# Kernel tuning notes

Measured on AMD Instinct MI355X. Metric: run time of the kernel, lower is better.

Reference implementation:

```python
import jax, jax.numpy as jnp
import numpy as np

PAD_IDX = 1  # matches init_kwargs pad_idx
TLEN, BATCH, D_IN = 50, 16, 512
SRC_LEN, VOCAB, CVOCAB = 200, 20000, 20400


def setup_inputs() -> dict:
    key = jax.random.key(0)
    k1, k2, k3, k4, k5, k6, k7 = jax.random.split(key, 7)
    hidden = jax.random.normal(k1, (TLEN, BATCH, D_IN), dtype=jnp.float32)
    attn = jax.random.uniform(k2, (TLEN, BATCH, SRC_LEN), dtype=jnp.float32)
    # src_map is a sparse one-hot indicator: each source position maps to one extended-vocab id
    src_ids = jax.random.randint(k3, (SRC_LEN, BATCH), 0, CVOCAB)
    src_map = jax.nn.one_hot(src_ids, CVOCAB, dtype=jnp.float32)  # (src_len, batch, cvocab)
    s = 1.0 / np.sqrt(D_IN)
    W = jax.random.uniform(k4, (VOCAB, D_IN), dtype=jnp.float32, minval=-s, maxval=s)
    b = jax.random.uniform(k5, (VOCAB,), dtype=jnp.float32, minval=-s, maxval=s)
    Wc = jax.random.uniform(k6, (1, D_IN), dtype=jnp.float32, minval=-s, maxval=s)
    bc = jax.random.uniform(k7, (1,), dtype=jnp.float32, minval=-s, maxval=s)
    return {"hidden": hidden, "attn": attn, "src_map": src_map, "W": W, "b": b, "Wc": Wc, "bc": bc}


def reference(hidden, attn, src_map, W, b, Wc, bc):
    tlen, batch, _ = hidden.shape
    src_len, _, cvocab = src_map.shape
    logits = jnp.einsum('tbd,vd->tbv', hidden, W) + b            # (tlen, batch, vocab)
    # faithful to torch: logits[:, pad_idx] = -inf (indexes the batch dim!)
    logits = logits.at[:, PAD_IDX, :].set(-jnp.inf)
    prob = jax.nn.softmax(logits, axis=1)                        # softmax over dim 1, as in source
    p_copy = jax.nn.sigmoid(jnp.einsum('tbd,od->tbo', hidden, Wc) + bc)  # (tlen, batch, 1)
    out_prob = prob * (1.0 - p_copy)                             # (tlen, batch, vocab)
    mul_attn = attn * p_copy                                     # (tlen, batch, src_len)
    # bmm over batch with one-hot src_map: effectively a scatter-add into extended vocab
    copy_prob = jnp.einsum('tbs,sbv->tbv', mul_attn, src_map)    # (tlen, batch, cvocab)
    # faithful to the split/stack/transpose permutation in the source
    flat = copy_prob.reshape(tlen * batch, cvocab)
    copy_prob = flat.reshape(batch, tlen, cvocab).swapaxes(0, 1) # (tlen, batch, cvocab)
    copy_prob = copy_prob.at[:, :, :out_prob.shape[2]].add(out_prob)
    return copy_prob
```

## Files before the change

kernel.cpp:

```cpp
#include <hip/hip_runtime.h>
#include <cstdint>
#include <cstddef>

#define TLEN    50
#define BATCH   16
#define D_IN    512
#define SRC_LEN 200
#define VOCAB   20000
#define CVOCAB  20400

typedef __bf16 bf16x8 __attribute__((ext_vector_type(8)));
typedef float  f32x4  __attribute__((ext_vector_type(4)));

#define GEMM_BLOCKS 625
#define ZERO_BLOCKS 40
#define SCAN_BLOCKS (SRC_LEN * BATCH)
#define NT 128
#define APAD 8

__global__ __launch_bounds__(256)
void pc_kernel(const float* __restrict__ hidden,
               const float* __restrict__ Wc,
               const float* __restrict__ bc,
               float* __restrict__ pc)
{
    const int row  = blockIdx.x * 4 + (threadIdx.x >> 6);
    const int lane = threadIdx.x & 63;
    const float* h = hidden + (size_t)row * D_IN + lane * 8;
    float4 h0 = *(const float4*)(h);
    float4 h1 = *(const float4*)(h + 4);
    float4 w0 = *(const float4*)(Wc + lane * 8);
    float4 w1 = *(const float4*)(Wc + lane * 8 + 4);
    float s = h0.x*w0.x + h0.y*w0.y + h0.z*w0.z + h0.w*w0.w
            + h1.x*w1.x + h1.y*w1.y + h1.z*w1.z + h1.w*w1.w;
    #pragma unroll
    for (int o = 1; o < 64; o <<= 1) s += __shfl_xor(s, o);
    if (lane == 0) pc[row] = 1.0f / (1.0f + __expf(-(s + bc[0])));
}

__global__ __launch_bounds__(NT)
void fused_main(const float* __restrict__ hidden,
                const float* __restrict__ src_map,
                const float* __restrict__ W,
                const float* __restrict__ pc,
                float* __restrict__ out,
                int* __restrict__ src_ids)
{
    const int bid = blockIdx.x;
    const int tid = threadIdx.x;

    if (bid < GEMM_BLOCKS) {
        __shared__ __bf16 Alds[2][BATCH][D_IN + APAD];

        const int lane = tid & 63;
        const int wv   = tid >> 6;
        const int l15  = lane & 15;
        const int q    = lane >> 4;
        const int colbase = bid * 32 + wv * 16;

        bf16x8 bfrag[16];
        {
            const float* wrow = W + (size_t)(colbase + l15) * D_IN + q * 8;
            #pragma unroll
            for (int c = 0; c < 16; ++c) {
                float4 f0 = *(const float4*)(wrow + c * 32);
                float4 f1 = *(const float4*)(wrow + c * 32 + 4);
                bf16x8 bf;
                bf[0] = (__bf16)f0.x; bf[1] = (__bf16)f0.y;
                bf[2] = (__bf16)f0.z; bf[3] = (__bf16)f0.w;
                bf[4] = (__bf16)f1.x; bf[5] = (__bf16)f1.y;
                bf[6] = (__bf16)f1.z; bf[7] = (__bf16)f1.w;
                bfrag[c] = bf;
            }
            #pragma unroll
            for (int c = 0; c < 16; ++c) {
                f32x4 t = *(f32x4*)&bfrag[c];
                asm volatile("" : "+v"(t));
                bfrag[c] = *(bf16x8*)&t;
            }
        }

        auto stage = [&](int t, int buf) {
            #pragma unroll
            for (int i = 0; i < 16; ++i) {
                float4 v4 = *(const float4*)(hidden + ((size_t)t * BATCH + i) * D_IN + tid * 4);
                __bf16* dst = &Alds[buf][i][tid * 4];
                dst[0] = (__bf16)v4.x; dst[1] = (__bf16)v4.y;
                dst[2] = (__bf16)v4.z; dst[3] = (__bf16)v4.w;
            }
        };

        stage(0, 0);

        for (int t = 0; t < TLEN; ++t) {
            __syncthreads();
            if (t + 1 < TLEN) stage(t + 1, (t + 1) & 1);

            const __bf16* arow = &Alds[t & 1][l15][q * 8];
            f32x4 accA = {0.f, 0.f, 0.f, 0.f};
            f32x4 accB = {0.f, 0.f, 0.f, 0.f};
            #pragma unroll
            for (int c = 0; c < 16; c += 2) {
                bf16x8 a0 = *(const bf16x8*)(arow + c * 32);
                bf16x8 a1 = *(const bf16x8*)(arow + c * 32 + 32);
                accA = __builtin_amdgcn_mfma_f32_16x16x32_bf16(a0, bfrag[c],     accA, 0, 0, 0);
                accB = __builtin_amdgcn_mfma_f32_16x16x32_bf16(a1, bfrag[c + 1], accB, 0, 0, 0);
            }
            f32x4 acc = accA + accB;

            float4 pc4 = *(const float4*)(pc + t * 16 + q * 4);

            float mx = -INFINITY;
            #pragma unroll
            for (int r = 0; r < 4; ++r)
                if (q * 4 + r != 1) mx = fmaxf(mx, acc[r]);
            mx = fmaxf(mx, __shfl_xor(mx, 16));
            mx = fmaxf(mx, __shfl_xor(mx, 32));
            float e[4], s = 0.f;
            #pragma unroll
            for (int r = 0; r < 4; ++r) {
                e[r] = (q * 4 + r == 1) ? 0.f : __expf(acc[r] - mx);
                s += e[r];
            }
            s += __shfl_xor(s, 16);
            s += __shfl_xor(s, 32);
            const float inv = 1.0f / s;
            const int v = colbase + l15;
            #pragma unroll
            for (int r = 0; r < 4; ++r) {
                const int b = q * 4 + r;
                out[(size_t)(t * BATCH + b) * CVOCAB + v] = e[r] * inv * (1.0f - pc4[r]);
            }
        }
    } else if (bid < GEMM_BLOCKS + ZERO_BLOCKS) {
        const int zb = bid - GEMM_BLOCKS;
        const float4 z = {0.f, 0.f, 0.f, 0.f};
        for (int i = tid; i < 2000; i += NT) {
            const int f = zb * 2000 + i;
            const int r = f / 100;
            const int c = f % 100;
            *(float4*)(out + (size_t)r * CVOCAB + VOCAB + c * 4) = z;
        }
    } else {
        const int row = bid - GEMM_BLOCKS - ZERO_BLOCKS;
        const float4* base = (const float4*)(src_map + (size_t)row * CVOCAB);
        int found = -1;
        for (int i0 = tid; i0 < 1275; i0 += NT) {
            float4 x0 = base[i0];
            float4 x1 = base[i0 + 1275];
            float4 x2 = base[i0 + 2550];
            float4 x3 = base[i0 + 3825];
            #pragma unroll
            for (int seg = 0; seg < 4; ++seg) {
                float4 x = seg == 0 ? x0 : seg == 1 ? x1 : seg == 2 ? x2 : x3;
                const int e0 = (i0 + seg * 1275) * 4;
                if (x.x > 0.5f) found = e0;
                if (x.y > 0.5f) found = e0 + 1;
                if (x.z > 0.5f) found = e0 + 2;
                if (x.w > 0.5f) found = e0 + 3;
            }
        }
        if (found >= 0) src_ids[row] = found;
    }
}

__global__ __launch_bounds__(256)
void scatter_copy(const float* __restrict__ attn,
                  const float* __restrict__ pc,
                  const int* __restrict__ src_ids,
                  float* __restrict__ out)
{
    const int p  = blockIdx.x;
    const int si = threadIdx.x;
    if (si >= SRC_LEN) return;
    const int b  = p & 15;
    const size_t obase = (size_t)((p % TLEN) * BATCH + (p / TLEN)) * CVOCAB;
    const int id = src_ids[si * BATCH + b];
    const float val = attn[(size_t)p * SRC_LEN + si] * pc[p];
    if ((unsigned)id < (unsigned)CVOCAB)
        atomicAdd(out + obase + id, val);
}

extern "C" void kernel_launch(void* const* d_in, const int* in_sizes, int n_in,
                              void* d_out, int out_size, void* d_ws, size_t ws_size,
                              hipStream_t stream)
{
    const float* hidden  = (const float*)d_in[0];
    const float* attn    = (const float*)d_in[1];
    const float* src_map = (const float*)d_in[2];
    const float* W       = (const float*)d_in[3];
    const float* Wc      = (const float*)d_in[5];
    const float* bc      = (const float*)d_in[6];
    float* out   = (float*)d_out;
    int* src_ids = (int*)d_ws;
    float* pc    = (float*)d_ws + 3200;

    pc_kernel<<<dim3(200), dim3(256), 0, stream>>>(hidden, Wc, bc, pc);
    fused_main<<<dim3(GEMM_BLOCKS + ZERO_BLOCKS + SCAN_BLOCKS), dim3(NT), 0, stream>>>(
        hidden, src_map, W, pc, out, src_ids);
    scatter_copy<<<dim3(TLEN * BATCH), dim3(256), 0, stream>>>(attn, pc, src_ids, out);
}
```

Before: 439.7 us.

## Pre-convert hidden to bf16 and stage tiles via direct global-to-LDS loads with swizzle

After: 428.6 us, median of 2. 2.5% less time.

```diff
diff --git a/kernel.cpp b/kernel.cpp
--- a/kernel.cpp
+++ b/kernel.cpp
@@ -16,30 +16,46 @@
 #define ZERO_BLOCKS 40
 #define SCAN_BLOCKS (SRC_LEN * BATCH)
 #define NT 128
-#define APAD 8
+
+typedef __attribute__((address_space(3))) uint32_t lds_t;
+typedef const __attribute__((address_space(1))) uint32_t glb_t;
 
 __global__ __launch_bounds__(256)
-void pc_kernel(const float* __restrict__ hidden,
-               const float* __restrict__ Wc,
-               const float* __restrict__ bc,
-               float* __restrict__ pc)
-{
-    const int row  = blockIdx.x * 4 + (threadIdx.x >> 6);
-    const int lane = threadIdx.x & 63;
-    const float* h = hidden + (size_t)row * D_IN + lane * 8;
-    float4 h0 = *(const float4*)(h);
-    float4 h1 = *(const float4*)(h + 4);
-    float4 w0 = *(const float4*)(Wc + lane * 8);
-    float4 w1 = *(const float4*)(Wc + lane * 8 + 4);
-    float s = h0.x*w0.x + h0.y*w0.y + h0.z*w0.z + h0.w*w0.w
-            + h1.x*w1.x + h1.y*w1.y + h1.z*w1.z + h1.w*w1.w;
-    #pragma unroll
-    for (int o = 1; o < 64; o <<= 1) s += __shfl_xor(s, o);
-    if (lane == 0) pc[row] = 1.0f / (1.0f + __expf(-(s + bc[0])));
+void prep_kernel(const float* __restrict__ hidden,
+                 const float* __restrict__ Wc,
+                 const float* __restrict__ bc,
+                 float* __restrict__ pc,
+                 __bf16* __restrict__ hb)
+{
+    const int bid = blockIdx.x;
+    if (bid < 200) {
+        const int row  = bid * 4 + (threadIdx.x >> 6);
+        const int lane = threadIdx.x & 63;
+        const float* h = hidden + (size_t)row * D_IN + lane * 8;
+        float4 h0 = *(const float4*)(h);
+        float4 h1 = *(const float4*)(h + 4);
+        float4 w0 = *(const float4*)(Wc + lane * 8);
+        float4 w1 = *(const float4*)(Wc + lane * 8 + 4);
+        float s = h0.x*w0.x + h0.y*w0.y + h0.z*w0.z + h0.w*w0.w
+                + h1.x*w1.x + h1.y*w1.y + h1.z*w1.z + h1.w*w1.w;
+        #pragma unroll
+        for (int o = 1; o < 64; o <<= 1) s += __shfl_xor(s, o);
+        if (lane == 0) pc[row] = 1.0f / (1.0f + __expf(-(s + bc[0])));
+    } else {
+        const int e = ((bid - 200) * 256 + threadIdx.x) * 8;
+        float4 f0 = *(const float4*)(hidden + e);
+        float4 f1 = *(const float4*)(hidden + e + 4);
+        bf16x8 bf;
+        bf[0] = (__bf16)f0.x; bf[1] = (__bf16)f0.y;
+        bf[2] = (__bf16)f0.z; bf[3] = (__bf16)f0.w;
+        bf[4] = (__bf16)f1.x; bf[5] = (__bf16)f1.y;
+        bf[6] = (__bf16)f1.z; bf[7] = (__bf16)f1.w;
+        *(bf16x8*)(hb + e) = bf;
+    }
 }
 
 __global__ __launch_bounds__(NT)
-void fused_main(const float* __restrict__ hidden,
+void fused_main(const __bf16* __restrict__ hb,
                 const float* __restrict__ src_map,
                 const float* __restrict__ W,
                 const float* __restrict__ pc,
@@ -50,7 +66,7 @@
     const int tid = threadIdx.x;
 
     if (bid < GEMM_BLOCKS) {
-        __shared__ __bf16 Alds[2][BATCH][D_IN + APAD];
+        __shared__ __bf16 Alds[2][BATCH][D_IN];
 
         const int lane = tid & 63;
         const int wv   = tid >> 6;
@@ -80,29 +96,40 @@
             }
         }
 
+        int jsrc[8];
+        #pragma unroll
+        for (int r = 0; r < 8; ++r) {
+            const int j = r * 128 + tid;
+            jsrc[r] = (j ^ ((j >> 6) & 7)) << 4;
+        }
+        const char* hbb  = (const char*)hb;
+        char* lbase = (char*)&Alds[0][0][0];
+
         auto stage = [&](int t, int buf) {
-            #pragma unroll
-            for (int i = 0; i < 16; ++i) {
-                float4 v4 = *(const float4*)(hidden + ((size_t)t * BATCH + i) * D_IN + tid * 4);
-                __bf16* dst = &Alds[buf][i][tid * 4];
-                dst[0] = (__bf16)v4.x; dst[1] = (__bf16)v4.y;
-                dst[2] = (__bf16)v4.z; dst[3] = (__bf16)v4.w;
-            }
+            const char* gt = hbb + (size_t)t * (BATCH * D_IN * 2);
+            char* lb = lbase + buf * 16384 + wv * 1024;
+            #pragma unroll
+            for (int r = 0; r < 8; ++r)
+                __builtin_amdgcn_global_load_lds((glb_t*)(gt + jsrc[r]),
+                                                 (lds_t*)(lb + r * 2048),
+                                                 16, 0, 0);
         };
 
         stage(0, 0);
+
+        const int xr = (l15 & 7) << 4;
 
         for (int t = 0; t < TLEN; ++t) {
             __syncthreads();
             if (t + 1 < TLEN) stage(t + 1, (t + 1) & 1);
 
-            const __bf16* arow = &Alds[t & 1][l15][q * 8];
+            const char* arow = lbase + (t & 1) * 16384 + l15 * 1024;
             f32x4 accA = {0.f, 0.f, 0.f, 0.f};
             f32x4 accB = {0.f, 0.f, 0.f, 0.f};
             #pragma unroll
             for (int c = 0; c < 16; c += 2) {
-                bf16x8 a0 = *(const bf16x8*)(arow + c * 32);
-                bf16x8 a1 = *(const bf16x8*)(arow + c * 32 + 32);
+                bf16x8 a0 = *(const bf16x8*)(arow + ((c * 64      + q * 16) ^ xr));
+                bf16x8 a1 = *(const bf16x8*)(arow + ((c * 64 + 64 + q * 16) ^ xr));
                 accA = __builtin_amdgcn_mfma_f32_16x16x32_bf16(a0, bfrag[c],     accA, 0, 0, 0);
                 accB = __builtin_amdgcn_mfma_f32_16x16x32_bf16(a1, bfrag[c + 1], accB, 0, 0, 0);
             }
@@ -170,13 +197,13 @@
                   const int* __restrict__ src_ids,
                   float* __restrict__ out)
 {
-    const int p  = blockIdx.x;
-    const int si = threadIdx.x;
-    if (si >= SRC_LEN) return;
+    const int w  = blockIdx.x * 256 + threadIdx.x;
+    const int p  = w / SRC_LEN;
+    const int si = w - p * SRC_LEN;
     const int b  = p & 15;
     const size_t obase = (size_t)((p % TLEN) * BATCH + (p / TLEN)) * CVOCAB;
     const int id = src_ids[si * BATCH + b];
-    const float val = attn[(size_t)p * SRC_LEN + si] * pc[p];
+    const float val = attn[w] * pc[p];
     if ((unsigned)id < (unsigned)CVOCAB)
         atomicAdd(out + obase + id, val);
 }
@@ -192,11 +219,13 @@
     const float* Wc      = (const float*)d_in[5];
     const float* bc      = (const float*)d_in[6];
     float* out   = (float*)d_out;
-    int* src_ids = (int*)d_ws;
-    float* pc    = (float*)d_ws + 3200;
-
-    pc_kernel<<<dim3(200), dim3(256), 0, stream>>>(hidden, Wc, bc, pc);
+
+    __bf16* hb   = (__bf16*)d_ws;
+    int* src_ids = (int*)((char*)d_ws + 819200);
+    float* pc    = (float*)((char*)d_ws + 819200 + 12800);
+
+    prep_kernel<<<dim3(400), dim3(256), 0, stream>>>(hidden, Wc, bc, pc, hb);
     fused_main<<<dim3(GEMM_BLOCKS + ZERO_BLOCKS + SCAN_BLOCKS), dim3(NT), 0, stream>>>(
-        hidden, src_map, W, pc, out, src_ids);
-    scatter_copy<<<dim3(TLEN * BATCH), dim3(256), 0, stream>>>(attn, pc, src_ids, out);
-}
+        hb, src_map, W, pc, out, src_ids);
+    scatter_copy<<<dim3(625), dim3(256), 0, stream>>>(attn, pc, src_ids, out);
+}
```
